# Kernel tuning notes

Hardware: AMD Instinct MI355X
Metric: run time of the kernel (lower is better)

The kernel has to match this reference:

```python
import jax, jax.numpy as jnp
import numpy as np

D_MODEL = 1024
N_HEADS = 16
D_HEAD = D_MODEL // N_HEADS
GN_EPS = 1e-5


def setup_inputs() -> dict:
    key = jax.random.key(0)
    ks = jax.random.split(key, 5)
    B, T = 2, 2048
    s = 1.0 / np.sqrt(D_MODEL)
    x = jax.random.normal(ks[0], (B, T, D_MODEL), dtype=jnp.float32)
    W_q = jax.random.normal(ks[1], (D_MODEL, D_MODEL), dtype=jnp.float32) * s
    W_k = jax.random.normal(ks[2], (D_MODEL, D_MODEL), dtype=jnp.float32) * s
    W_v = jax.random.normal(ks[3], (D_MODEL, D_MODEL), dtype=jnp.float32) * s
    W_o = jax.random.normal(ks[4], (D_MODEL, D_MODEL), dtype=jnp.float32) * s
    gn_weight = jnp.ones((D_MODEL,), dtype=jnp.float32)
    gn_bias = jnp.zeros((D_MODEL,), dtype=jnp.float32)
    return {"x": x, "W_q": W_q, "W_k": W_k, "W_v": W_v, "W_o": W_o,
            "gn_weight": gn_weight, "gn_bias": gn_bias}


def reference(x, W_q, W_k, W_v, W_o, gn_weight, gn_bias):
    B, T, _ = x.shape
    H, Dh = N_HEADS, D_HEAD
    # Projections (nn.Linear: y = x @ W.T), split heads -> [B, T, H, Dh]
    q = (x @ W_q.T).reshape(B, T, H, Dh)
    k = (x @ W_k.T).reshape(B, T, H, Dh)
    v = (x @ W_v.T).reshape(B, T, H, Dh)

    # Per-head causal decay mask D_h[i, j] = gamma_h^(i-j) for i >= j else 0
    gammas = jnp.asarray([1.0 - 2.0 ** (-5.0 - i) for i in range(H)],
                         dtype=jnp.float32)  # [H]
    idx = jnp.arange(T, dtype=jnp.float32)
    diff = idx[:, None] - idx[None, :]  # [T, T]
    decay = jnp.where(diff >= 0,
                      gammas[:, None, None] ** jnp.maximum(diff, 0.0),
                      0.0)  # [H, T, T]

    scale = jnp.sqrt(jnp.asarray(Dh, dtype=x.dtype))
    qk = jnp.einsum('bthd,bshd->bhts', q, k)          # [B, H, T, T]
    attn = qk * decay[None] / scale
    y = jnp.einsum('bhts,bshd->bthd', attn, v)        # [B, T, H, Dh]

    # GroupNorm(n_heads groups) over channels-last-transposed layout:
    # torch applies it to [B, d_model, T]; each group = one head's Dh channels,
    # normalized over (Dh, T).
    yg = y.transpose(0, 2, 3, 1)                      # [B, H, Dh, T]
    mean = yg.mean(axis=(2, 3), keepdims=True)
    var = yg.var(axis=(2, 3), keepdims=True)
    yn = (yg - mean) / jnp.sqrt(var + GN_EPS)
    yn = yn * gn_weight.reshape(1, H, Dh, 1) + gn_bias.reshape(1, H, Dh, 1)
    y = yn.transpose(0, 3, 1, 2).reshape(B, T, H * Dh)  # [B, T, d_model]
    return y @ W_o.T
```

## Files before the change

### kernel.cpp

```cpp
#include <hip/hip_runtime.h>
#include <math.h>

#define TSEQ 2048
#define NB   2
#define DM   1024
#define NH   16
#define DH   64
#define GN_EPS 1e-5f

typedef short v8s __attribute__((ext_vector_type(8)));
typedef short v4s __attribute__((ext_vector_type(4)));
typedef float v4f __attribute__((ext_vector_type(4)));

__device__ __forceinline__ short f2bf(float f) {
    union { float f; unsigned u; } c; c.f = f;
    unsigned u = c.u;
    unsigned r = (u + 0x7fffu + ((u >> 16) & 1u)) >> 16;
    return (short)r;
}
__device__ __forceinline__ float bf2f(short s) {
    union { unsigned u; float f; } c; c.u = ((unsigned)(unsigned short)s) << 16;
    return c.f;
}

__device__ __forceinline__ unsigned cvtpk_bf16(float lo, float hi) {
    unsigned r;
    asm("v_cvt_pk_bf16_f32 %0, %1, %2" : "=v"(r) : "v"(lo), "v"(hi));
    return r;
}

__device__ __forceinline__ void gl_lds16(const void* g, void* l) {
    __builtin_amdgcn_global_load_lds(
        (const __attribute__((address_space(1))) void*)g,
        (__attribute__((address_space(3))) void*)l, 16, 0, 0);
}

__global__ __launch_bounds__(256) void cast_kernel(
    const float* __restrict__ x,
    const float* __restrict__ Wq, const float* __restrict__ Wk,
    const float* __restrict__ Wv, const float* __restrict__ Wo,
    short* __restrict__ xbf, short* __restrict__ wbf)
{
    const int NX = NB * TSEQ * DM;
    const int NW = DM * DM;
    const int total4 = (NX + 4 * NW) / 4;
    for (int i = blockIdx.x * 256 + threadIdx.x; i < total4;
         i += gridDim.x * 256) {
        int e = i * 4;
        const float* src; short* dst;
        if (e < NX) { src = x + e; dst = xbf + e; }
        else {
            int o = e - NX;
            int w = o >> 20;
            int r = o & (NW - 1);
            src = (w == 0 ? Wq : w == 1 ? Wk : w == 2 ? Wv : Wo) + r;
            dst = wbf + o;
        }
        v4f v = *(const v4f*)src;
        v4s s;
        #pragma unroll
        for (int j = 0; j < 4; ++j) s[j] = f2bf(v[j]);
        *(v4s*)dst = s;
    }
}

__global__ __launch_bounds__(256, 2) void gemm_qkv_fused(
    const short* __restrict__ xbf, const short* __restrict__ wbf,
    short* __restrict__ Qb, short* __restrict__ Kb,
    short* __restrict__ Kt, short* __restrict__ Vt)
{
    const int bid = blockIdx.x;
    const int xcd = bid & 7, ch = bid >> 3;
    const int sm = xcd >> 1, sn = xcd & 1;
    const int m0 = (sm * 8 + (ch >> 3)) * 128;
    const int n0 = (sn * 8 + (ch & 7)) * 64;

    const int t = threadIdx.x, l = t & 63, w = t >> 6;
    const int wm = (w >> 1) * 64, wn = (w & 1) * 32;
    const int lr = l & 15, g = l >> 4;
    const int swz = (lr & 7) << 4;

    __shared__ short As[128 * 64];
    __shared__ short Bs[3][64 * 64];

    v4f acc[3][4][2];
    #pragma unroll
    for (int z = 0; z < 3; ++z)
        #pragma unroll
        for (int i = 0; i < 4; ++i)
            #pragma unroll
            for (int j = 0; j < 2; ++j) acc[z][i][j] = (v4f){0.f,0.f,0.f,0.f};

    const char* Agp = (const char*)(xbf + (size_t)m0 * DM);
    const char* Bgp = (const char*)(wbf + (size_t)n0 * DM);
    const size_t ZS = (size_t)DM * DM * 2;

    int soffA[4], sdstA[4], soffB[2], sdstB[2];
    #pragma unroll
    for (int p = 0; p < 4; ++p) {
        int c = p * 256 + t;
        int row = c >> 3, u = c & 7;
        soffA[p] = row * (DM * 2) + ((u * 16) ^ ((row & 7) << 4));
        sdstA[p] = (p * 256 + (t & 192)) * 16;
    }
    #pragma unroll
    for (int p = 0; p < 2; ++p) {
        int c = p * 256 + t;
        int row = c >> 3, u = c & 7;
        soffB[p] = row * (DM * 2) + ((u * 16) ^ ((row & 7) << 4));
        sdstB[p] = (p * 256 + (t & 192)) * 16;
    }

    for (int kt = 0; kt < DM / 64; ++kt) {
        const int kb = kt * 128;
        #pragma unroll
        for (int p = 0; p < 4; ++p)
            gl_lds16(Agp + (size_t)soffA[p] + kb, (char*)As + sdstA[p]);
        #pragma unroll
        for (int z = 0; z < 3; ++z)
            #pragma unroll
            for (int p = 0; p < 2; ++p)
                gl_lds16(Bgp + ZS * z + (size_t)soffB[p] + kb,
                         (char*)Bs[z] + sdstB[p]);
        asm volatile("s_waitcnt vmcnt(0)" ::: "memory");
        __syncthreads();

        v8s af[4][2];
        #pragma unroll
        for (int i = 0; i < 4; ++i) {
            int rowa = wm + i * 16 + lr;
            af[i][0] = *(const v8s*)((const char*)As + rowa * 128 + ((g * 16) ^ swz));
            af[i][1] = *(const v8s*)((const char*)As + rowa * 128 + ((64 + g * 16) ^ swz));
        }
        #pragma unroll
        for (int z = 0; z < 3; ++z) {
            #pragma unroll
            for (int j = 0; j < 2; ++j) {
                int rowb = wn + j * 16 + lr;
                v8s b0 = *(const v8s*)((const char*)Bs[z] + rowb * 128 + ((g * 16) ^ swz));
                v8s b1 = *(const v8s*)((const char*)Bs[z] + rowb * 128 + ((64 + g * 16) ^ swz));
                #pragma unroll
                for (int i = 0; i < 4; ++i) {
                    if (z == 0) {
                        acc[0][i][j] = __builtin_amdgcn_mfma_f32_16x16x32_bf16(
                            b0, af[i][0], acc[0][i][j], 0, 0, 0);
                        acc[0][i][j] = __builtin_amdgcn_mfma_f32_16x16x32_bf16(
                            b1, af[i][1], acc[0][i][j], 0, 0, 0);
                    } else {
                        acc[z][i][j] = __builtin_amdgcn_mfma_f32_16x16x32_bf16(
                            af[i][0], b0, acc[z][i][j], 0, 0, 0);
                        acc[z][i][j] = __builtin_amdgcn_mfma_f32_16x16x32_bf16(
                            af[i][1], b1, acc[z][i][j], 0, 0, 0);
                    }
                }
            }
        }
        __syncthreads();
    }

    const int head = n0 >> 6;
    const float l2g = log2f(1.0f - exp2f(-5.0f - (float)head));

    {
        float fac[4];
        #pragma unroll
        for (int i = 0; i < 4; ++i) {
            int tl = (m0 + wm + i * 16 + lr) & 63;
            fac[i] = exp2f(fmaf(l2g, (float)tl, -3.0f));
        }
        #pragma unroll
        for (int i = 0; i < 4; ++i) {
            int mrow = m0 + wm + i * 16 + lr;
            #pragma unroll
            for (int j = 0; j < 2; ++j) {
                int ncol = n0 + wn + j * 16 + g * 4;
                v4s pk;
                #pragma unroll
                for (int r = 0; r < 4; ++r) pk[r] = f2bf(acc[0][i][j][r] * fac[i]);
                *(v4s*)(Qb + (size_t)mrow * DM + ncol) = pk;
            }
        }
    }
    {
        const float l2gk = -l2g;
        #pragma unroll
        for (int i = 0; i < 4; ++i) {
            int row  = m0 + wm + i * 16 + g * 4;
            int bidx = row >> 11, tb = row & (TSEQ - 1);
            #pragma unroll
            for (int j = 0; j < 2; ++j) {
                int col = n0 + wn + j * 16 + lr;
                v4s pk;
                #pragma unroll
                for (int r = 0; r < 4; ++r) {
                    int tl = (row + r) & 63;
                    float fc = exp2f(l2gk * (float)tl);
                    short bv = f2bf(acc[1][i][j][r] * fc);
                    Kb[(size_t)(row + r) * DM + col] = bv;
                    pk[r] = bv;
                }
                *(v4s*)(Kt + ((size_t)bidx << 21) + ((size_t)col << 11) + tb) = pk;
            }
        }
    }
    {
        #pragma unroll
        for (int i = 0; i < 4; ++i) {
            int row  = m0 + wm + i * 16 + g * 4;
            int bidx = row >> 11, tb = row & (TSEQ - 1);
            #pragma unroll
            for (int j = 0; j < 2; ++j) {
                int col = n0 + wn + j * 16 + lr;
                v4s pk;
                #pragma unroll
                for (int r = 0; r < 4; ++r) pk[r] = f2bf(acc[2][i][j][r]);
                *(v4s*)(Vt + ((size_t)bidx << 21) + ((size_t)col << 11) + tb) = pk;
            }
        }
    }
}

template <bool SWAP>
__device__ __forceinline__ void mm_loop_db(
    const char* Agp, const char* Bgp, char* lds,
    int t, int lr, int g, int wr, int wc, v4f acc[4][4])
{
    int soff[4], sdst[4];
    #pragma unroll
    for (int p = 0; p < 4; ++p) {
        int i = p * 256 + t;
        int row = i >> 3;
        int cp  = (i & 7) * 16;
        soff[p] = row * (DM * 2) + (cp ^ ((row & 7) << 4));
        sdst[p] = (p * 256 + (t & 192)) * 16;
    }
    const int swz = (lr & 7) << 4;

    #pragma unroll
    for (int p = 0; p < 4; ++p) {
        gl_lds16(Agp + (size_t)soff[p], lds + sdst[p]);
        gl_lds16(Bgp + (size_t)soff[p], lds + 16384 + sdst[p]);
    }

    for (int kt = 0; kt < DM / 64; ++kt) {
        const char* cur = lds + (kt & 1) * 32768;
        asm volatile("s_waitcnt vmcnt(0)" ::: "memory");
        __syncthreads();

        if (kt < DM / 64 - 1) {
            char* nxt = lds + ((kt + 1) & 1) * 32768;
            const int kb = (kt + 1) * 128;
            #pragma unroll
            for (int p = 0; p < 4; ++p) {
                gl_lds16(Agp + (size_t)soff[p] + kb, nxt + sdst[p]);
                gl_lds16(Bgp + (size_t)soff[p] + kb, nxt + 16384 + sdst[p]);
            }
        }

        v8s bfr[4][2];
        #pragma unroll
        for (int j = 0; j < 4; ++j) {
            int rowb = wc + j * 16 + lr;
            #pragma unroll
            for (int ks = 0; ks < 2; ++ks)
                bfr[j][ks] = *(const v8s*)(cur + 16384 + rowb * 128
                               + ((ks * 64 + g * 16) ^ swz));
        }
        #pragma unroll
        for (int i = 0; i < 4; ++i) {
            int rowa = wr + i * 16 + lr;
            v8s a0 = *(const v8s*)(cur + rowa * 128 + ((g * 16) ^ swz));
            v8s a1 = *(const v8s*)(cur + rowa * 128 + ((64 + g * 16) ^ swz));
            #pragma unroll
            for (int j = 0; j < 4; ++j) {
                if (SWAP) {
                    acc[i][j] = __builtin_amdgcn_mfma_f32_16x16x32_bf16(
                        bfr[j][0], a0, acc[i][j], 0, 0, 0);
                    acc[i][j] = __builtin_amdgcn_mfma_f32_16x16x32_bf16(
                        bfr[j][1], a1, acc[i][j], 0, 0, 0);
                } else {
                    acc[i][j] = __builtin_amdgcn_mfma_f32_16x16x32_bf16(
                        a0, bfr[j][0], acc[i][j], 0, 0, 0);
                    acc[i][j] = __builtin_amdgcn_mfma_f32_16x16x32_bf16(
                        a1, bfr[j][1], acc[i][j], 0, 0, 0);
                }
            }
        }
    }
}

__global__ __launch_bounds__(256, 2) void chunk_kv(
    const short* __restrict__ Kt, const short* __restrict__ Vt,
    short* __restrict__ At)
{
    const int bid = blockIdx.x;
    const int c = bid & 31, bh = bid >> 5;
    const int b = bh >> 4, h = bh & 15;
    const int tid = threadIdx.x, l = tid & 63, w = tid >> 6;
    const int lr = l & 15, g = l >> 4;

    const size_t rowbase = ((size_t)b * DM + h * 64);

    v8s kf[2], vf[4][2];
    {
        const short* kp = Kt + (rowbase + 16 * w + lr) * TSEQ + 64 * c;
        kf[0] = *(const v8s*)(kp + g * 8);
        kf[1] = *(const v8s*)(kp + 32 + g * 8);
    }
    #pragma unroll
    for (int j = 0; j < 4; ++j) {
        const short* vp = Vt + (rowbase + j * 16 + lr) * TSEQ + 64 * c;
        vf[j][0] = *(const v8s*)(vp + g * 8);
        vf[j][1] = *(const v8s*)(vp + 32 + g * 8);
    }

    v4f acc[4];
    #pragma unroll
    for (int j = 0; j < 4; ++j) acc[j] = (v4f){0.f, 0.f, 0.f, 0.f};

    #pragma unroll
    for (int j = 0; j < 4; ++j) {
        acc[j] = __builtin_amdgcn_mfma_f32_16x16x32_bf16(kf[0], vf[j][0], acc[j], 0, 0, 0);
        acc[j] = __builtin_amdgcn_mfma_f32_16x16x32_bf16(kf[1], vf[j][1], acc[j], 0, 0, 0);
    }

    short* Ab = At + (((size_t)bh * 32 + c) << 12);
    #pragma unroll
    for (int j = 0; j < 4; ++j) {
        v4s pk;
        #pragma unroll
        for (int r = 0; r < 4; ++r) pk[r] = f2bf(acc[j][r]);
        *(v4s*)(Ab + (j * 16 + lr) * 64 + 16 * w + g * 4) = pk;
    }
}

__global__ __launch_bounds__(256) void chunk_scan(
    const short* __restrict__ At, short* __restrict__ St)
{
    const int idx = blockIdx.x * 256 + threadIdx.x;
    const int bh = idx >> 12;
    const int h  = bh & 15;
    const float l2g = log2f(1.0f - exp2f(-5.0f - (float)h));
    const float g64 = exp2f(l2g * 64.0f);

    const size_t base = ((size_t)bh << 17) + (idx & 4095);
    float state = 0.0f;
    #pragma unroll
    for (int c = 1; c < 32; ++c) {
        float a = bf2f(At[base + ((size_t)(c - 1) << 12)]);
        state = g64 * (state + a);
        St[base + ((size_t)c << 12)] = f2bf(state);
    }
}

__global__ __launch_bounds__(256, 2) void chunk_out(
    const short* __restrict__ Qb, const short* __restrict__ Kb,
    const short* __restrict__ Vt, const short* __restrict__ St,
    short* __restrict__ Ybf, float* __restrict__ psums)
{
    const int bid = blockIdx.x;
    const int xcd = bid & 7, r8 = bid >> 3;
    const int bh  = xcd * 4 + (r8 >> 5);
    const int c   = r8 & 31;
    const int b = bh >> 4, h = bh & 15;
    const int tid = threadIdx.x, l = tid & 63, w = tid >> 6;
    const int lr = l & 15, g = l >> 4;

    __shared__ short strip[64 * 64];
    __shared__ float tr[64][68];
    __shared__ float red[8];

    const size_t rowQK = ((size_t)(b * TSEQ + 64 * c)) * DM + h * 64;

    v8s qf[4][2];
    #pragma unroll
    for (int j = 0; j < 4; ++j) {
        const short* qp = Qb + rowQK + (size_t)(j * 16 + lr) * DM;
        qf[j][0] = *(const v8s*)(qp + g * 8);
        qf[j][1] = *(const v8s*)(qp + 32 + g * 8);
    }
    v8s kf0, kf1;
    {
        const short* kp = Kb + rowQK + (size_t)(16 * w + lr) * DM;
        kf0 = *(const v8s*)(kp + g * 8);
        kf1 = *(const v8s*)(kp + 32 + g * 8);
    }
    v8s sf0 = {}, sf1 = {};
    if (c > 0) {
        const short* sp = St + (((size_t)bh * 32 + c) << 12) + (16 * w + lr) * 64;
        sf0 = *(const v8s*)(sp + g * 8);
        sf1 = *(const v8s*)(sp + 32 + g * 8);
    }
    v8s vf0, vf1;
    {
        const short* vp = Vt + ((size_t)(b * DM + h * 64) + 16 * w + lr) * TSEQ
                          + 64 * c;
        vf0 = *(const v8s*)(vp + g * 8);
        vf1 = *(const v8s*)(vp + 32 + g * 8);
    }

    v4f s[4];
    #pragma unroll
    for (int j = 0; j < 4; ++j) {
        v4f a = (v4f){0.f, 0.f, 0.f, 0.f};
        a = __builtin_amdgcn_mfma_f32_16x16x32_bf16(kf0, qf[j][0], a, 0, 0, 0);
        a = __builtin_amdgcn_mfma_f32_16x16x32_bf16(kf1, qf[j][1], a, 0, 0, 0);
        s[j] = a;
    }

    v4f y[4];
    #pragma unroll
    for (int j = 0; j < 4; ++j) y[j] = (v4f){0.f, 0.f, 0.f, 0.f};
    if (c > 0) {
        #pragma unroll
        for (int j = 0; j < 4; ++j) {
            y[j] = __builtin_amdgcn_mfma_f32_16x16x32_bf16(sf0, qf[j][0], y[j], 0, 0, 0);
            y[j] = __builtin_amdgcn_mfma_f32_16x16x32_bf16(sf1, qf[j][1], y[j], 0, 0, 0);
        }
    }

    #pragma unroll
    for (int j = 0; j < 4; ++j) {
        v4f vv = s[j];
        #pragma unroll
        for (int r = 0; r < 4; ++r)
            if ((j * 16 + lr) - (16 * w + g * 4 + r) < 0) vv[r] = 0.0f;
        unsigned u0 = cvtpk_bf16(vv[0], vv[1]);
        unsigned u1 = cvtpk_bf16(vv[2], vv[3]);
        int byte = ((j * 16 + lr) * 128 + 32 * w + g * 8) ^ ((lr & 7) << 4);
        *(unsigned long long*)((char*)strip + byte) =
            (unsigned long long)u0 | ((unsigned long long)u1 << 32);
    }
    __syncthreads();

    #pragma unroll
    for (int j = 0; j < 4; ++j) {
        int rb = (j * 16 + lr) * 128;
        int sw = (lr & 7) << 4;
        v8s sB0 = *(const v8s*)((char*)strip + ((rb + g * 16) ^ sw));
        v8s sB1 = *(const v8s*)((char*)strip + ((rb + 64 + g * 16) ^ sw));
        y[j] = __builtin_amdgcn_mfma_f32_16x16x32_bf16(vf0, sB0, y[j], 0, 0, 0);
        y[j] = __builtin_amdgcn_mfma_f32_16x16x32_bf16(vf1, sB1, y[j], 0, 0, 0);
    }

    float lsum = 0.f, lsq = 0.f;
    #pragma unroll
    for (int j = 0; j < 4; ++j)
        #pragma unroll
        for (int r = 0; r < 4; ++r) {
            float vy = y[j][r];
            lsum += vy; lsq += vy * vy;
        }
    #pragma unroll
    for (int m = 32; m; m >>= 1) {
        lsum += __shfl_xor(lsum, m, 64);
        lsq  += __shfl_xor(lsq,  m, 64);
    }
    if (l == 0) { red[w] = lsum; red[4 + w] = lsq; }

    #pragma unroll
    for (int j = 0; j < 4; ++j)
        #pragma unroll
        for (int r = 0; r < 4; ++r)
            tr[j * 16 + lr][16 * w + g * 4 + r] = y[j][r];
    __syncthreads();

    if (tid == 0) {
        float* ps = psums + ((size_t)bh * 32 + c) * 2;
        ps[0] = red[0] + red[1] + red[2] + red[3];
        ps[1] = red[4] + red[5] + red[6] + red[7];
    }

    #pragma unroll
    for (int u = 0; u < 4; ++u) {
        int row  = (tid >> 4) + u * 16;
        int col4 = (tid & 15) * 4;
        v4f val = *(const v4f*)&tr[row][col4];
        v4s pk;
        #pragma unroll
        for (int r = 0; r < 4; ++r) pk[r] = f2bf(val[r]);
        *(v4s*)&Ybf[(size_t)(b * TSEQ + 64 * c + row) * DM + h * 64 + col4] = pk;
    }
}

__global__ __launch_bounds__(256) void gn_finalize(
    const float* __restrict__ psums,
    const float* __restrict__ gnw, const float* __restrict__ gnb,
    float* __restrict__ scale, float* __restrict__ shift)
{
    int idx = blockIdx.x * 256 + threadIdx.x;
    if (idx >= NB * DM) return;
    int bb = idx >> 10;
    int ch = idx & (DM - 1);
    int hh = ch >> 6;
    int bh = bb * 16 + hh;

    float s = 0.f, q = 0.f;
    #pragma unroll
    for (int k = 0; k < 32; ++k) {
        s += psums[((size_t)bh * 32 + k) * 2];
        q += psums[((size_t)bh * 32 + k) * 2 + 1];
    }
    const float n = (float)(DH * TSEQ);
    float mean = s / n;
    float var  = q / n - mean * mean;
    float rstd = rsqrtf(var + GN_EPS);
    float sc = rstd * gnw[ch];
    scale[idx] = sc;
    shift[idx] = gnb[ch] - mean * sc;
}

__global__ __launch_bounds__(256) void wo_prep(
    const short* __restrict__ Wob, const float* __restrict__ scale,
    const float* __restrict__ shift,
    short* __restrict__ Wo2, float* __restrict__ bias)
{
    const int tid = threadIdx.x, l = tid & 63, w = tid >> 6;
    const int bn = blockIdx.x * 4 + w;
    const int b = bn >> 10, n = bn & 1023;
    const int k0 = l * 16;

    const short* wp = Wob + (size_t)n * DM + k0;
    v8s w0 = *(const v8s*)wp;
    v8s w1 = *(const v8s*)(wp + 8);
    const float* sc = scale + b * DM + k0;
    const float* sh = shift + b * DM + k0;

    v8s o0, o1;
    float bsum = 0.f;
    #pragma unroll
    for (int j = 0; j < 8; ++j) {
        float wf = bf2f(w0[j]);
        o0[j] = f2bf(wf * sc[j]);
        bsum = fmaf(sh[j], wf, bsum);
    }
    #pragma unroll
    for (int j = 0; j < 8; ++j) {
        float wf = bf2f(w1[j]);
        o1[j] = f2bf(wf * sc[8 + j]);
        bsum = fmaf(sh[8 + j], wf, bsum);
    }
    short* op = Wo2 + ((size_t)b * DM + n) * DM + k0;
    *(v8s*)op = o0;
    *(v8s*)(op + 8) = o1;

    #pragma unroll
    for (int m = 32; m; m >>= 1) bsum += __shfl_xor(bsum, m, 64);
    if (l == 0) bias[bn] = bsum;
}

__global__ __launch_bounds__(256, 2) void gemm_out_mfma(
    const short* __restrict__ Ybf, const short* __restrict__ Wo2,
    const float* __restrict__ bias, float* __restrict__ out)
{
    const int bid = blockIdx.x;
    const int swizb = (bid & 7) * 32 + (bid >> 3);
    const int n0 = (swizb & 7) * 128, m0 = (swizb >> 3) * 128;
    const int b = m0 >> 11;
    const int t = threadIdx.x, l = t & 63, w = t >> 6;
    const int wr = (w >> 1) * 64, wc = (w & 1) * 64;
    const int lr = l & 15, g = l >> 4;

    __shared__ char lds[65536];

    v4f acc[4][4];
    #pragma unroll
    for (int i = 0; i < 4; ++i)
        #pragma unroll
        for (int j = 0; j < 4; ++j) acc[i][j] = (v4f){0.f, 0.f, 0.f, 0.f};

    const char* Agp = (const char*)(Ybf + (size_t)m0 * DM);
    const char* Bgp = (const char*)(Wo2 + (size_t)b * DM * DM + (size_t)n0 * DM);

    mm_loop_db<true>(Agp, Bgp, lds, t, lr, g, wr, wc, acc);

    #pragma unroll
    for (int i = 0; i < 4; ++i) {
        int mrow = m0 + wr + i * 16 + lr;
        #pragma unroll
        for (int j = 0; j < 4; ++j) {
            int ncol = n0 + wc + j * 16 + g * 4;
            v4f bv = *(const v4f*)&bias[b * DM + ncol];
            v4f o = acc[i][j] + bv;
            *(v4f*)&out[(size_t)mrow * DM + ncol] = o;
        }
    }
}

extern "C" void kernel_launch(void* const* d_in, const int* in_sizes, int n_in,
                              void* d_out, int out_size, void* d_ws, size_t ws_size,
                              hipStream_t stream)
{
    const float* x   = (const float*)d_in[0];
    const float* Wq  = (const float*)d_in[1];
    const float* Wk  = (const float*)d_in[2];
    const float* Wv  = (const float*)d_in[3];
    const float* Wo  = (const float*)d_in[4];
    const float* gnw = (const float*)d_in[5];
    const float* gnb = (const float*)d_in[6];
    float* out = (float*)d_out;

    char* wsb = (char*)d_ws;
    size_t o = 0;
    short* Qb   = (short*)(wsb + o); o += (size_t)NB * TSEQ * DM * 2;
    short* Kb   = (short*)(wsb + o); o += (size_t)NB * TSEQ * DM * 2;
    short* Kt   = (short*)(wsb + o); o += (size_t)NB * TSEQ * DM * 2;
    short* Vt   = (short*)(wsb + o); o += (size_t)NB * TSEQ * DM * 2;
    short* xbf  = (short*)(wsb + o); o += (size_t)NB * TSEQ * DM * 2;
    short* wbf  = (short*)(wsb + o); o += (size_t)4 * DM * DM * 2;
    short* Ybf  = (short*)(wsb + o); o += (size_t)NB * TSEQ * DM * 2;
    short* St   = (short*)(wsb + o); o += (size_t)NB * TSEQ * DM * 2;
    short* Wo2  = (short*)(wsb + o); o += (size_t)NB * DM * DM * 2;
    float* psums = (float*)(wsb + o); o += (size_t)32 * 32 * 2 * 4;
    float* scale = (float*)(wsb + o); o += (size_t)NB * DM * 4;
    float* shift = (float*)(wsb + o); o += (size_t)NB * DM * 4;
    float* bias  = (float*)(wsb + o); o += (size_t)NB * DM * 4;
    if (ws_size < o) return;

    short* At = xbf;

    cast_kernel<<<2048, 256, 0, stream>>>(x, Wq, Wk, Wv, Wo, xbf, wbf);
    gemm_qkv_fused<<<dim3(512), 256, 0, stream>>>(xbf, wbf, Qb, Kb, Kt, Vt);
    chunk_kv<<<dim3(1024), 256, 0, stream>>>(Kt, Vt, At);
    chunk_scan<<<dim3(512), 256, 0, stream>>>(At, St);
    chunk_out<<<dim3(1024), 256, 0, stream>>>(Qb, Kb, Vt, St, Ybf, psums);
    gn_finalize<<<dim3((NB * DM + 255) / 256), 256, 0, stream>>>(
        psums, gnw, gnb, scale, shift);
    wo_prep<<<dim3(512), 256, 0, stream>>>(
        wbf + 3 * (size_t)DM * DM, scale, shift, Wo2, bias);
    gemm_out_mfma<<<dim3(256), 256, 0, stream>>>(Ybf, Wo2, bias, out);
}
```

Baseline: 88.17 us.

## Double-buffer LDS tiles in fused QKV GEMM to overlap loads with MFMA

Replaces the single A/B shared-memory tiles in the fused QKV projection GEMM with two 40KB buffers. The next k-tile's global-to-LDS loads are issued right after the barrier, so they overlap with the MFMA work on the current tile, and the trailing barrier is dropped. This aims to hide global memory latency that previously stalled every iteration. LDS per block doubles to 80KB, which could limit occupancy at the requested two blocks per CU.

```diff
diff --git a/kernel.cpp b/kernel.cpp
--- a/kernel.cpp
+++ b/kernel.cpp
@@ -80,8 +80,7 @@
     const int lr = l & 15, g = l >> 4;
     const int swz = (lr & 7) << 4;
 
-    __shared__ short As[128 * 64];
-    __shared__ short Bs[3][64 * 64];
+    __shared__ char lds[81920];
 
     v4f acc[3][4][2];
     #pragma unroll
@@ -111,34 +110,43 @@
         sdstB[p] = (p * 256 + (t & 192)) * 16;
     }
 
+#define STAGE(tt) { \
+    char* base_ = lds + ((tt) & 1) * 40960; \
+    const size_t kb_ = (size_t)(tt) * 128; \
+    _Pragma("unroll") \
+    for (int p = 0; p < 4; ++p) \
+        gl_lds16(Agp + (size_t)soffA[p] + kb_, base_ + sdstA[p]); \
+    _Pragma("unroll") \
+    for (int z = 0; z < 3; ++z) \
+        _Pragma("unroll") \
+        for (int p = 0; p < 2; ++p) \
+            gl_lds16(Bgp + ZS * z + (size_t)soffB[p] + kb_, \
+                     base_ + 16384 + z * 8192 + sdstB[p]); }
+
+    STAGE(0);
+
     for (int kt = 0; kt < DM / 64; ++kt) {
-        const int kb = kt * 128;
-        #pragma unroll
-        for (int p = 0; p < 4; ++p)
-            gl_lds16(Agp + (size_t)soffA[p] + kb, (char*)As + sdstA[p]);
-        #pragma unroll
-        for (int z = 0; z < 3; ++z)
-            #pragma unroll
-            for (int p = 0; p < 2; ++p)
-                gl_lds16(Bgp + ZS * z + (size_t)soffB[p] + kb,
-                         (char*)Bs[z] + sdstB[p]);
+        const char* cur = lds + (kt & 1) * 40960;
         asm volatile("s_waitcnt vmcnt(0)" ::: "memory");
         __syncthreads();
 
+        if (kt < DM / 64 - 1) STAGE(kt + 1);
+
         v8s af[4][2];
         #pragma unroll
         for (int i = 0; i < 4; ++i) {
             int rowa = wm + i * 16 + lr;
-            af[i][0] = *(const v8s*)((const char*)As + rowa * 128 + ((g * 16) ^ swz));
-            af[i][1] = *(const v8s*)((const char*)As + rowa * 128 + ((64 + g * 16) ^ swz));
+            af[i][0] = *(const v8s*)(cur + rowa * 128 + ((g * 16) ^ swz));
+            af[i][1] = *(const v8s*)(cur + rowa * 128 + ((64 + g * 16) ^ swz));
         }
         #pragma unroll
         for (int z = 0; z < 3; ++z) {
+            const char* Bz = cur + 16384 + z * 8192;
             #pragma unroll
             for (int j = 0; j < 2; ++j) {
                 int rowb = wn + j * 16 + lr;
-                v8s b0 = *(const v8s*)((const char*)Bs[z] + rowb * 128 + ((g * 16) ^ swz));
-                v8s b1 = *(const v8s*)((const char*)Bs[z] + rowb * 128 + ((64 + g * 16) ^ swz));
+                v8s b0 = *(const v8s*)(Bz + rowb * 128 + ((g * 16) ^ swz));
+                v8s b1 = *(const v8s*)(Bz + rowb * 128 + ((64 + g * 16) ^ swz));
                 #pragma unroll
                 for (int i = 0; i < 4; ++i) {
                     if (z == 0) {
@@ -155,8 +163,8 @@
                 }
             }
         }
-        __syncthreads();
-    }
+    }
+#undef STAGE
 
     const int head = n0 >> 6;
     const float l2g = log2f(1.0f - exp2f(-5.0f - (float)head));
```

New measurement: 86.83 us. Within noise of the previous version (-1.5%).
